# Performance work log

Hardware: AMD Instinct MI355X
Metric: run time of the kernel (lower is better)

The kernel has to match this reference:

```python
import jax, jax.numpy as jnp
import numpy as np
from jax import lax

PATCH = 8

def setup_inputs() -> dict:
    key = jax.random.key(0)
    ks = jax.random.split(key, 9)
    B, C, H, W = 16, 1, 128, 128
    return {
        "x": jax.random.normal(ks[0], (B, C, H, W), jnp.float32),
        "wq": jax.random.normal(ks[1], (1, 1), jnp.float32),
        "bq": jax.random.normal(ks[2], (1,), jnp.float32),
        "wk": jax.random.normal(ks[3], (1, 1), jnp.float32),
        "bk": jax.random.normal(ks[4], (1,), jnp.float32),
        "wv": jax.random.normal(ks[5], (1, 1), jnp.float32),
        "bv": jax.random.normal(ks[6], (1,), jnp.float32),
        "conv_w": jax.random.normal(ks[7], (1, 1, PATCH, PATCH), jnp.float32) * 0.1,
        "conv_b": jax.random.normal(ks[8], (1,), jnp.float32),
    }

def reference(x, wq, bq, wk, bk, wv, bv, conv_w, conv_b):
    B, C, H, W = x.shape
    # spatial-reduction projection: Conv2d(1,1,k=p,stride=p)
    ds = lax.conv_general_dilated(
        x, conv_w, window_strides=(PATCH, PATCH), padding="VALID",
        dimension_numbers=("NCHW", "OIHW", "NCHW")) + conv_b[None, :, None, None]
    b, c, h, w = ds.shape
    down = ds.reshape(b, c, h * w).transpose(0, 2, 1)      # [B, hw, 1]
    x_ = x.reshape(B, C, H * W).transpose(0, 2, 1)          # [B, HW, 1]
    q = x_ @ wq.T + bq                                      # [B, HW, 1]
    k = down @ wk.T + bk                                    # [B, hw, 1]
    v = down @ wv.T + bv                                    # [B, hw, 1]
    qk = jnp.einsum("bqd,bkd->bqk", q, k)                  # [B, HW, hw] (unscaled)
    attn = jax.nn.softmax(qk, axis=-1)
    out = jnp.einsum("bqk,bkd->bqd", attn, v)              # [B, HW, 1]
    return out.reshape(B, 1, H, W)
```

## Files before the change

kernel.cpp:

```cpp
#include <hip/hip_runtime.h>

#define PATCH 8
#define BATCH 16
#define H 128
#define W 128
#define HW (H * W)
#define NK 256
#define BLOCKS_PER_BATCH 64

__global__ __launch_bounds__(256) void gsa_kernel(
    const float* __restrict__ x,
    const float* __restrict__ wq, const float* __restrict__ bq,
    const float* __restrict__ wk, const float* __restrict__ bk,
    const float* __restrict__ wv, const float* __restrict__ bv,
    const float* __restrict__ conv_w, const float* __restrict__ conv_b,
    float* __restrict__ out)
{
    __shared__ float k_lds[NK];
    __shared__ float v_lds[NK];
    __shared__ float cw[64];
    __shared__ float red[8];

    const int tid   = threadIdx.x;
    const int b     = blockIdx.x >> 6;
    const int chunk = blockIdx.x & 63;

    if (tid < 64) cw[tid] = conv_w[tid];
    __syncthreads();

    const int ph = tid >> 4;
    const int pw = tid & 15;
    const float* xb = x + b * HW;
    const float* pbase = xb + (ph * PATCH) * W + pw * PATCH;

    float ds = 0.f;
    #pragma unroll
    for (int r = 0; r < PATCH; ++r) {
        const float4 a0 = *reinterpret_cast<const float4*>(pbase + r * W);
        const float4 a1 = *reinterpret_cast<const float4*>(pbase + r * W + 4);
        const float* cr = &cw[r * 8];
        ds = fmaf(a0.x, cr[0], ds); ds = fmaf(a0.y, cr[1], ds);
        ds = fmaf(a0.z, cr[2], ds); ds = fmaf(a0.w, cr[3], ds);
        ds = fmaf(a1.x, cr[4], ds); ds = fmaf(a1.y, cr[5], ds);
        ds = fmaf(a1.z, cr[6], ds); ds = fmaf(a1.w, cr[7], ds);
    }
    ds += conv_b[0];

    const float kj = fmaf(ds, wk[0], bk[0]);
    const float vj = fmaf(ds, wv[0], bv[0]);
    k_lds[tid] = kj;
    v_lds[tid] = vj;

    float kmax = kj, kmin = kj;
    #pragma unroll
    for (int off = 32; off > 0; off >>= 1) {
        kmax = fmaxf(kmax, __shfl_xor(kmax, off));
        kmin = fminf(kmin, __shfl_xor(kmin, off));
    }
    const int wave = tid >> 6;
    if ((tid & 63) == 0) { red[wave] = kmax; red[4 + wave] = kmin; }
    __syncthreads();
    kmax = fmaxf(fmaxf(red[0], red[1]), fmaxf(red[2], red[3]));
    kmin = fminf(fminf(red[4], red[5]), fminf(red[6], red[7]));

    const int i = chunk * 256 + tid;
    const float LOG2E = 1.4426950408889634f;
    const float ql = fmaf(xb[i], wq[0], bq[0]) * LOG2E;
    const float ml = fmaxf(ql * kmax, ql * kmin);

    float sum = 0.f, acc = 0.f;
    #pragma unroll 8
    for (int j = 0; j < NK; ++j) {
        const float e = exp2f(fmaf(ql, k_lds[j], -ml));
        sum += e;
        acc = fmaf(e, v_lds[j], acc);
    }
    out[b * HW + i] = acc / sum;
}

extern "C" void kernel_launch(void* const* d_in, const int* in_sizes, int n_in,
                              void* d_out, int out_size, void* d_ws, size_t ws_size,
                              hipStream_t stream) {
    const float* x      = (const float*)d_in[0];
    const float* wq     = (const float*)d_in[1];
    const float* bq     = (const float*)d_in[2];
    const float* wk     = (const float*)d_in[3];
    const float* bk     = (const float*)d_in[4];
    const float* wv     = (const float*)d_in[5];
    const float* bv     = (const float*)d_in[6];
    const float* conv_w = (const float*)d_in[7];
    const float* conv_b = (const float*)d_in[8];
    float* out = (float*)d_out;

    dim3 grid(BATCH * BLOCKS_PER_BATCH);
    dim3 block(256);
    gsa_kernel<<<grid, block, 0, stream>>>(x, wq, bq, wk, bk, wv, bv,
                                           conv_w, conv_b, out);
}
```

Before: 89.09 us.

## Process two queries per thread with interleaved k/v float4 LDS and raw exp2

Halves the number of blocks so each thread handles two query pixels, which halves the per-block recomputation of the downsampled conv and the k/v reductions. K and V are interleaved into float4 LDS entries so one wide LDS read feeds four exponentials. Independent accumulators break the add dependency chains, and the hardware exp2 builtin replaces exp2f to skip range-handling code. The cost is fewer blocks (512) on a large GPU, which may leave compute units underused, and the raw exp2 may lose accuracy on denormal inputs.

```diff
diff --git a/kernel.cpp b/kernel.cpp
--- a/kernel.cpp
+++ b/kernel.cpp
@@ -6,7 +6,14 @@
 #define W 128
 #define HW (H * W)
 #define NK 256
-#define BLOCKS_PER_BATCH 64
+#define BLOCKS_PER_BATCH 32
+#define QPB 512
+
+#if __has_builtin(__builtin_amdgcn_exp2f)
+#define EXP2(x) __builtin_amdgcn_exp2f(x)
+#else
+#define EXP2(x) exp2f(x)
+#endif
 
 __global__ __launch_bounds__(256) void gsa_kernel(
     const float* __restrict__ x,
@@ -16,14 +23,13 @@
     const float* __restrict__ conv_w, const float* __restrict__ conv_b,
     float* __restrict__ out)
 {
-    __shared__ float k_lds[NK];
-    __shared__ float v_lds[NK];
+    __shared__ float4 kv4[NK / 2];
     __shared__ float cw[64];
     __shared__ float red[8];
 
     const int tid   = threadIdx.x;
-    const int b     = blockIdx.x >> 6;
-    const int chunk = blockIdx.x & 63;
+    const int b     = blockIdx.x >> 5;
+    const int chunk = blockIdx.x & 31;
 
     if (tid < 64) cw[tid] = conv_w[tid];
     __syncthreads();
@@ -48,8 +54,9 @@
 
     const float kj = fmaf(ds, wk[0], bk[0]);
     const float vj = fmaf(ds, wv[0], bv[0]);
-    k_lds[tid] = kj;
-    v_lds[tid] = vj;
+    float* kvf = reinterpret_cast<float*>(kv4);
+    kvf[(tid >> 1) * 4 + (tid & 1)]     = kj;
+    kvf[(tid >> 1) * 4 + 2 + (tid & 1)] = vj;
 
     float kmax = kj, kmin = kj;
     #pragma unroll
@@ -63,19 +70,33 @@
     kmax = fmaxf(fmaxf(red[0], red[1]), fmaxf(red[2], red[3]));
     kmin = fminf(fminf(red[4], red[5]), fminf(red[6], red[7]));
 
-    const int i = chunk * 256 + tid;
     const float LOG2E = 1.4426950408889634f;
-    const float ql = fmaf(xb[i], wq[0], bq[0]) * LOG2E;
-    const float ml = fmaxf(ql * kmax, ql * kmin);
+    const float wq0 = wq[0], bq0 = bq[0];
+    const int i0 = chunk * QPB + tid;
+    const int i1 = i0 + 256;
+    const float ql0 = fmaf(xb[i0], wq0, bq0) * LOG2E;
+    const float ql1 = fmaf(xb[i1], wq0, bq0) * LOG2E;
+    const float nml0 = -fmaxf(ql0 * kmax, ql0 * kmin);
+    const float nml1 = -fmaxf(ql1 * kmax, ql1 * kmin);
 
-    float sum = 0.f, acc = 0.f;
-    #pragma unroll 8
-    for (int j = 0; j < NK; ++j) {
-        const float e = exp2f(fmaf(ql, k_lds[j], -ml));
-        sum += e;
-        acc = fmaf(e, v_lds[j], acc);
+    float s0a = 0.f, s0b = 0.f, a0a = 0.f, a0b = 0.f;
+    float s1a = 0.f, s1b = 0.f, a1a = 0.f, a1b = 0.f;
+
+    #pragma unroll 4
+    for (int m = 0; m < NK / 2; ++m) {
+        const float4 t = kv4[m];
+        const float e00 = EXP2(fmaf(ql0, t.x, nml0));
+        const float e01 = EXP2(fmaf(ql0, t.y, nml0));
+        const float e10 = EXP2(fmaf(ql1, t.x, nml1));
+        const float e11 = EXP2(fmaf(ql1, t.y, nml1));
+        s0a += e00; a0a = fmaf(e00, t.z, a0a);
+        s0b += e01; a0b = fmaf(e01, t.w, a0b);
+        s1a += e10; a1a = fmaf(e10, t.z, a1a);
+        s1b += e11; a1b = fmaf(e11, t.w, a1b);
     }
-    out[b * HW + i] = acc / sum;
+
+    out[b * HW + i0] = (a0a + a0b) / (s0a + s0b);
+    out[b * HW + i1] = (a1a + a1b) / (s1a + s1b);
 }
 
 extern "C" void kernel_launch(void* const* d_in, const int* in_sizes, int n_in,
```

Measured after the change: 81.62 us. 8.4% less time.
